# Optimization experiments

Measured on AMD Instinct MI355X. Metric: run time of the kernel, lower is better.

The kernel has to match this reference:

```python
import jax, jax.numpy as jnp
import numpy as np

N, M, D = 32768, 4096, 128  # samples, SOM units (64x64), input_dim
GRID_H, GRID_W = 64, 64


def setup_inputs() -> dict:
    key = jax.random.key(0)
    k1, k2 = jax.random.split(key)
    inputs = jax.random.normal(k1, (N, D), dtype=jnp.float32)
    # SOM2D.__init__: weights = torch.rand(size, input_dim)
    weights = jax.random.uniform(k2, (M, D), dtype=jnp.float32)
    # grid = meshgrid(arange(H), arange(W)) -> [M, 2] integer unit coordinates
    gx, gy = jnp.meshgrid(jnp.arange(GRID_H), jnp.arange(GRID_W), indexing='ij')
    grid = jnp.stack([gx, gy], axis=-1).reshape(-1, 2).astype(jnp.int32)
    return {"inputs": inputs, "weights": weights, "grid": grid}


def reference(inputs, weights, grid):
    # sed(x, y): squared Euclidean distance [N, M].
    # tensor the torch code materializes; same math.
    x_sq = jnp.sum(inputs * inputs, axis=1, keepdims=True)        # [N, 1]
    w_sq = jnp.sum(weights * weights, axis=1)                      # [M]
    cross = jnp.einsum('nd,md->nm', inputs, weights)               # [N, M]
    distances = x_sq + w_sq - 2.0 * cross                          # [N, M]
    # wtac: argmin over units, then lookup grid coordinates of the winner.
    winning_indices = jnp.argmin(distances, axis=1)                # [N]
    winning_labels = grid[winning_indices]                         # [N, 2]
    return winning_labels
```

## Files before the change

kernel.cpp:

```cpp
#include <hip/hip_runtime.h>
#include <float.h>
#include <stdint.h>


constexpr int D = 128;

typedef _Float16 f16x8 __attribute__((ext_vector_type(8)));
typedef float    f32x4 __attribute__((ext_vector_type(4)));

__device__ __forceinline__ void cvt_split(const float4& a0, const float4& a1,
                                          f16x8& h, f16x8& l) {
    float v[8] = {a0.x, a0.y, a0.z, a0.w, a1.x, a1.y, a1.z, a1.w};
#pragma unroll
    for (int j = 0; j < 8; ++j) {
        _Float16 hh = (_Float16)v[j];
        h[j] = hh;
        l[j] = (_Float16)(v[j] - (float)hh);
    }
}

__global__ __launch_bounds__(256) void prep_kernel(
        const float* __restrict__ w, f16x8* __restrict__ hG,
        f16x8* __restrict__ lG, float* __restrict__ wsq, int M) {
    int g = blockIdx.x * 256 + threadIdx.x;
    if (g >= M * 16) return;
    int u = g >> 4, o = g & 15;
    const float4* wp = reinterpret_cast<const float4*>(w + (size_t)u * D + o * 8);
    float4 a0 = wp[0], a1 = wp[1];
    f16x8 h, l;
    cvt_split(a0, a1, h, l);
    float ss = 0.f;
    ss = fmaf(a0.x, a0.x, ss); ss = fmaf(a0.y, a0.y, ss);
    ss = fmaf(a0.z, a0.z, ss); ss = fmaf(a0.w, a0.w, ss);
    ss = fmaf(a1.x, a1.x, ss); ss = fmaf(a1.y, a1.y, ss);
    ss = fmaf(a1.z, a1.z, ss); ss = fmaf(a1.w, a1.w, ss);
#pragma unroll
    for (int m = 1; m < 16; m <<= 1) ss += __shfl_xor(ss, m, 64);
    if (o == 0) wsq[u] = ss;
    int slot = ((u >> 5) << 9) + ((o >> 2) << 7) + (((u >> 4) & 1) << 6)
             + ((o & 3) << 4) + (u & 15);
    hG[slot] = h;
    lG[slot] = l;
}

__global__ void finalize(const unsigned long long* __restrict__ keys,
                         const int* __restrict__ grid, int* __restrict__ out,
                         int N, int UG) {
    int s = blockIdx.x * blockDim.x + threadIdx.x;
    if (s >= N) return;
    unsigned long long k = keys[s];
    for (int g = 1; g < UG; ++g) {
        unsigned long long kg = keys[(size_t)g * N + s];
        if (kg < k) k = kg;
    }
    int idx = (int)(unsigned)(k & 0xFFFFFFFFull);
    out[2 * s]     = grid[2 * idx];
    out[2 * s + 1] = grid[2 * idx + 1];
}

template <bool PARTIAL>
__global__ __launch_bounds__(256, 2) void som_main(
        const float* __restrict__ x, const f16x8* __restrict__ hG,
        const f16x8* __restrict__ lG, const float* __restrict__ wsq,
        const int* __restrict__ grid, int* __restrict__ out,
        unsigned long long* __restrict__ keys,
        int unitGroups, int M, int N) {
    const int tid  = threadIdx.x;
    const int lane = tid & 63;
    const int wv   = tid >> 6;
    const int c    = lane & 15;
    const int q    = lane >> 4;

    const int ug    = blockIdx.x % unitGroups;
    const int sg    = blockIdx.x / unitGroups;
    const int sWave = sg * 256 + wv * 64;

    f16x8 Ah[16], Al[16];
#pragma unroll
    for (int i = 0; i < 4; ++i) {
        const float* xr = x + (size_t)(sWave + 16 * i + c) * D + q * 8;
#pragma unroll
        for (int s = 0; s < 4; ++s) {
            float4 a0 = *reinterpret_cast<const float4*>(xr + 32 * s);
            float4 a1 = *reinterpret_cast<const float4*>(xr + 32 * s + 4);
            cvt_split(a0, a1, Ah[i * 4 + s], Al[i * 4 + s]);
        }
    }

    float bestD[16];
    int   bestI[16];
#pragma unroll
    for (int sl = 0; sl < 16; ++sl) { bestD[sl] = FLT_MAX; bestI[sl] = 0; }

    const int tilesPer = (M / 32) / unitGroups;
    const int tile0    = ug * tilesPer;

    for (int tt = 0; tt < tilesPer; ++tt) {
        const int tile = tile0 + tt;
        const f16x8* hp = hG + ((size_t)tile << 9) + lane;
        const f16x8* lp = lG + ((size_t)tile << 9) + lane;

        f32x4 acc[8];
#pragma unroll
        for (int f = 0; f < 8; ++f) acc[f] = (f32x4){0.f, 0.f, 0.f, 0.f};

#pragma unroll
        for (int s = 0; s < 4; ++s) {
            f16x8 bh[2], bl[2];
#pragma unroll
            for (int t = 0; t < 2; ++t) {
                bh[t] = hp[(size_t)(s * 128 + t * 64)];
                bl[t] = lp[(size_t)(s * 128 + t * 64)];
            }
#pragma unroll
            for (int i = 0; i < 4; ++i)
#pragma unroll
                for (int t = 0; t < 2; ++t)
                    acc[i * 2 + t] = __builtin_amdgcn_mfma_f32_16x16x32_f16(
                        Ah[i * 4 + s], bh[t], acc[i * 2 + t], 0, 0, 0);
#pragma unroll
            for (int i = 0; i < 4; ++i)
#pragma unroll
                for (int t = 0; t < 2; ++t)
                    acc[i * 2 + t] = __builtin_amdgcn_mfma_f32_16x16x32_f16(
                        Al[i * 4 + s], bh[t], acc[i * 2 + t], 0, 0, 0);
#pragma unroll
            for (int i = 0; i < 4; ++i)
#pragma unroll
                for (int t = 0; t < 2; ++t)
                    acc[i * 2 + t] = __builtin_amdgcn_mfma_f32_16x16x32_f16(
                        Ah[i * 4 + s], bl[t], acc[i * 2 + t], 0, 0, 0);
        }

        const int uTile = tile * 32;
#pragma unroll
        for (int t = 0; t < 2; ++t) {
            const int n    = uTile + 16 * t + c;
            const float wq = wsq[n];
#pragma unroll
            for (int i = 0; i < 4; ++i) {
                f32x4 a = acc[i * 2 + t];
#pragma unroll
                for (int r = 0; r < 4; ++r) {
                    float score = fmaf(-2.f, a[r], wq);
                    int sl = i * 4 + r;
                    if (score < bestD[sl]) { bestD[sl] = score; bestI[sl] = n; }
                }
            }
        }
    }

#pragma unroll
    for (int sl = 0; sl < 16; ++sl) {
        float d   = bestD[sl];
        int   idx = bestI[sl];
#pragma unroll
        for (int m = 1; m < 16; m <<= 1) {
            float od = __shfl_xor(d, m, 64);
            int   oi = __shfl_xor(idx, m, 64);
            if (od < d || (od == d && oi < idx)) { d = od; idx = oi; }
        }
        if (c == 0) {
            const int sOut = sWave + 16 * (sl >> 2) + 4 * q + (sl & 3);
            if (PARTIAL) {
                unsigned ub = __float_as_uint(d);
                ub = (ub & 0x80000000u) ? ~ub : (ub | 0x80000000u);
                unsigned long long key = ((unsigned long long)ub << 32) | (unsigned)idx;
                keys[(size_t)ug * N + sOut] = key;
            } else {
                out[2 * sOut]     = grid[2 * idx];
                out[2 * sOut + 1] = grid[2 * idx + 1];
            }
        }
    }
}

extern "C" void kernel_launch(void* const* d_in, const int* in_sizes, int n_in,
                              void* d_out, int out_size, void* d_ws, size_t ws_size,
                              hipStream_t stream) {
    const float* x    = (const float*)d_in[0];
    const float* w    = (const float*)d_in[1];
    const int*   grid = (const int*)d_in[2];
    int* out = (int*)d_out;

    const int N = in_sizes[0] / D;
    const int M = in_sizes[1] / D;

    const size_t hlBytes   = (size_t)M * D * 2;
    const size_t baseBytes = 2 * hlBytes + (size_t)M * 4;

    f16x8* hG  = (f16x8*)d_ws;
    f16x8* lG  = (f16x8*)((char*)d_ws + hlBytes);
    float* wsq = (float*)((char*)d_ws + 2 * hlBytes);
    unsigned long long* keys = (unsigned long long*)((char*)d_ws + baseBytes);

    prep_kernel<<<(M * 16 + 255) / 256, 256, 0, stream>>>(w, hG, lG, wsq, M);

    const int sampleGroups = N / 256;
    int UG = 0;
    if (ws_size >= baseBytes + 4ull * N * 8) UG = 4;
    else if (ws_size >= baseBytes + 2ull * N * 8) UG = 2;

    if (UG > 0) {
        som_main<true><<<sampleGroups * UG, 256, 0, stream>>>(
            x, hG, lG, wsq, grid, out, keys, UG, M, N);
        finalize<<<(N + 255) / 256, 256, 0, stream>>>(keys, grid, out, N, UG);
    } else {
        som_main<false><<<sampleGroups, 256, 0, stream>>>(
            x, hG, lG, wsq, grid, out, nullptr, 1, M, N);
    }
}
```

Before: 168.5 us.

## Move low-half input fragments to LDS and batch weight loads per tile

New measurement: 154.9 us (median of 2 runs). -8.1%, faster.

```diff
diff --git a/kernel.cpp b/kernel.cpp
--- a/kernel.cpp
+++ b/kernel.cpp
@@ -65,6 +65,8 @@
         const int* __restrict__ grid, int* __restrict__ out,
         unsigned long long* __restrict__ keys,
         int unitGroups, int M, int N) {
+    __shared__ f16x8 albuf[4 * 1024];
+
     const int tid  = threadIdx.x;
     const int lane = tid & 63;
     const int wv   = tid >> 6;
@@ -75,7 +77,9 @@
     const int sg    = blockIdx.x / unitGroups;
     const int sWave = sg * 256 + wv * 64;
 
-    f16x8 Ah[16], Al[16];
+    f16x8* myAl = &albuf[wv * 1024];
+
+    f16x8 Ah[16];
 #pragma unroll
     for (int i = 0; i < 4; ++i) {
         const float* xr = x + (size_t)(sWave + 16 * i + c) * D + q * 8;
@@ -83,7 +87,10 @@
         for (int s = 0; s < 4; ++s) {
             float4 a0 = *reinterpret_cast<const float4*>(xr + 32 * s);
             float4 a1 = *reinterpret_cast<const float4*>(xr + 32 * s + 4);
-            cvt_split(a0, a1, Ah[i * 4 + s], Al[i * 4 + s]);
+            f16x8 h, l;
+            cvt_split(a0, a1, h, l);
+            Ah[i * 4 + s] = h;
+            myAl[(i * 4 + s) * 64 + lane] = l;
         }
     }
 
@@ -100,43 +107,59 @@
         const f16x8* hp = hG + ((size_t)tile << 9) + lane;
         const f16x8* lp = lG + ((size_t)tile << 9) + lane;
 
+        f16x8 bh[8], bl[8];
+#pragma unroll
+        for (int s = 0; s < 4; ++s)
+#pragma unroll
+            for (int t = 0; t < 2; ++t)
+                bh[s * 2 + t] = hp[s * 128 + t * 64];
+#pragma unroll
+        for (int s = 0; s < 4; ++s)
+#pragma unroll
+            for (int t = 0; t < 2; ++t)
+                bl[s * 2 + t] = lp[s * 128 + t * 64];
+
+        const int uTile = tile * 32;
+        const float wq0 = wsq[uTile + c];
+        const float wq1 = wsq[uTile + 16 + c];
+
         f32x4 acc[8];
 #pragma unroll
         for (int f = 0; f < 8; ++f) acc[f] = (f32x4){0.f, 0.f, 0.f, 0.f};
 
 #pragma unroll
-        for (int s = 0; s < 4; ++s) {
-            f16x8 bh[2], bl[2];
-#pragma unroll
-            for (int t = 0; t < 2; ++t) {
-                bh[t] = hp[(size_t)(s * 128 + t * 64)];
-                bl[t] = lp[(size_t)(s * 128 + t * 64)];
-            }
+        for (int s = 0; s < 4; ++s)
 #pragma unroll
             for (int i = 0; i < 4; ++i)
 #pragma unroll
                 for (int t = 0; t < 2; ++t)
                     acc[i * 2 + t] = __builtin_amdgcn_mfma_f32_16x16x32_f16(
-                        Ah[i * 4 + s], bh[t], acc[i * 2 + t], 0, 0, 0);
+                        Ah[i * 4 + s], bh[s * 2 + t], acc[i * 2 + t], 0, 0, 0);
+#pragma unroll
+        for (int s = 0; s < 4; ++s) {
+            f16x8 al[4];
+#pragma unroll
+            for (int i = 0; i < 4; ++i) al[i] = myAl[(i * 4 + s) * 64 + lane];
 #pragma unroll
             for (int i = 0; i < 4; ++i)
 #pragma unroll
                 for (int t = 0; t < 2; ++t)
                     acc[i * 2 + t] = __builtin_amdgcn_mfma_f32_16x16x32_f16(
-                        Al[i * 4 + s], bh[t], acc[i * 2 + t], 0, 0, 0);
+                        al[i], bh[s * 2 + t], acc[i * 2 + t], 0, 0, 0);
+        }
+#pragma unroll
+        for (int s = 0; s < 4; ++s)
 #pragma unroll
             for (int i = 0; i < 4; ++i)
 #pragma unroll
                 for (int t = 0; t < 2; ++t)
                     acc[i * 2 + t] = __builtin_amdgcn_mfma_f32_16x16x32_f16(
-                        Ah[i * 4 + s], bl[t], acc[i * 2 + t], 0, 0, 0);
-        }
-
-        const int uTile = tile * 32;
+                        Ah[i * 4 + s], bl[s * 2 + t], acc[i * 2 + t], 0, 0, 0);
+
 #pragma unroll
         for (int t = 0; t < 2; ++t) {
             const int n    = uTile + 16 * t + c;
-            const float wq = wsq[n];
+            const float wq = t == 0 ? wq0 : wq1;
 #pragma unroll
             for (int i = 0; i < 4; ++i) {
                 f32x4 a = acc[i * 2 + t];
```
